# Optimization experiments

Measured on AMD Instinct MI355X. Metric: run time of the kernel, lower is better.

Reference implementation:

```python
import jax, jax.numpy as jnp
import numpy as np
from jax import lax

T = 8192
OBS = 512
HID = 2048
NOBJ = 8


def setup_inputs() -> dict:
    key = jax.random.key(0)
    ks = jax.random.split(key, 9)
    s_in = 1.0 / np.sqrt(OBS)
    s_hid = 1.0 / np.sqrt(HID)
    return {
        "x": jax.random.normal(ks[0], (T, OBS), dtype=jnp.float32),
        "W_in": jax.random.normal(ks[1], (HID, OBS), dtype=jnp.float32) * s_in,
        "W_B": jax.random.normal(ks[2], (HID, OBS), dtype=jnp.float32) * s_in,
        "W_C": jax.random.normal(ks[3], (HID, OBS), dtype=jnp.float32) * s_in,
        "W_delta": jax.random.normal(ks[4], (HID, OBS), dtype=jnp.float32) * s_in,
        "A_log": jax.random.normal(ks[5], (HID,), dtype=jnp.float32),
        "W_out": jax.random.normal(ks[6], (NOBJ, HID), dtype=jnp.float32) * s_hid,
        "b_out": jnp.zeros((NOBJ,), dtype=jnp.float32),
        "W_skip": jax.random.normal(ks[7], (NOBJ, OBS), dtype=jnp.float32) * s_in,
    }


def reference(x, W_in, W_B, W_C, W_delta, A_log, W_out, b_out, W_skip):
    # Input-dependent SSM parameters (4 GEMMs, [T, HID] each)
    x_state = x @ W_in.T
    B = x @ W_B.T
    C = x @ W_C.T
    delta = jax.nn.sigmoid(x @ W_delta.T)
    A = -jnp.exp(A_log)                      # [HID]

    A_bar = jnp.exp(delta * A)               # [T, HID], per-step decay
    Bx = B * x_state                         # [T, HID], per-step input

    def step(h, inp):
        a, bx = inp
        h = a * h + bx
        return h, h

    h0 = jnp.zeros((HID,), dtype=x.dtype)
    _, h_seq = lax.scan(step, h0, (A_bar, Bx))  # [T, HID]

    y = C * h_seq
    out = y @ W_out.T + b_out + x @ W_skip.T    # [T, NOBJ]
    return out
```

## Files before the change

### kernel.cpp

```cpp
#include <hip/hip_runtime.h>
#include <hip/hip_bf16.h>
#include <cstdint>

#define TT   8192
#define KOBS 512
#define HID  2048
#define NOBJ 8
#define NCH  64
#define CT   128

typedef unsigned short u16;
typedef uint32_t u32;
typedef short bf16x8 __attribute__((ext_vector_type(8)));
typedef float f32x4  __attribute__((ext_vector_type(4)));
typedef unsigned short u16x4 __attribute__((ext_vector_type(4)));

static __device__ __forceinline__ float bf2f(u16 u) {
    union { uint32_t i; float f; } v;
    v.i = ((uint32_t)u) << 16;
    return v.f;
}
static __device__ __forceinline__ u16 f2bf(float f) {
    union { float f; uint32_t i; } v;
    v.f = f;
    uint32_t lsb = (v.i >> 16) & 1u;
    uint32_t r = v.i + 0x7fffu + lsb;
    return (u16)(r >> 16);
}

static __device__ __forceinline__ void async_ld16(const u16* g, u16* l) {
    __builtin_amdgcn_global_load_lds(
        (const __attribute__((address_space(1))) uint32_t*)g,
        (__attribute__((address_space(3))) uint32_t*)l,
        16, 0, 0);
}

__global__ void prep_kernel(const float* __restrict__ x,
                            const float* __restrict__ Win,
                            const float* __restrict__ WB,
                            const float* __restrict__ WC,
                            const float* __restrict__ Wd,
                            const float* __restrict__ A_log,
                            u16* __restrict__ x_bf,
                            u16* __restrict__ W_bf,
                            float* __restrict__ A_e)
{
    const int tid0   = blockIdx.x * blockDim.x + threadIdx.x;
    const int stride = gridDim.x * blockDim.x;

    const float4* x4 = (const float4*)x;
    for (int i = tid0; i < TT * KOBS / 4; i += stride) {
        float4 v = x4[i];
        u16x4 o = { f2bf(v.x), f2bf(v.y), f2bf(v.z), f2bf(v.w) };
        *(u16x4*)&x_bf[(size_t)i * 4] = o;
    }

    for (int i = tid0; i < 4 * HID * KOBS / 8; i += stride) {
        int n  = i >> 6;
        int k8 = (i & 63) * 8;
        int h  = n >> 2;
        int w  = n & 3;
        const float* src = (w == 0) ? Win : (w == 1) ? WB : (w == 2) ? WC : Wd;
        const float4* s4 = (const float4*)(src + (size_t)h * KOBS + k8);
        float4 a = s4[0], b = s4[1];
        u16x4 o1 = { f2bf(a.x), f2bf(a.y), f2bf(a.z), f2bf(a.w) };
        u16x4 o2 = { f2bf(b.x), f2bf(b.y), f2bf(b.z), f2bf(b.w) };
        *(u16x4*)&W_bf[(size_t)i * 8]     = o1;
        *(u16x4*)&W_bf[(size_t)i * 8 + 4] = o2;
    }

    if (tid0 < HID)
        A_e[tid0] = -__expf(A_log[tid0]) * 1.44269504f;
}

__launch_bounds__(256)
__global__ void init_out(const float* __restrict__ x,
                         const float* __restrict__ b_out,
                         const float* __restrict__ W_skip,
                         float* __restrict__ out)
{
    const int wave = threadIdx.x >> 6;
    const int lane = threadIdx.x & 63;
    const int t0 = (blockIdx.x * 4 + wave) * 4;

    float acc[4][NOBJ];
#pragma unroll
    for (int tt = 0; tt < 4; tt++)
#pragma unroll
        for (int o = 0; o < NOBJ; o++) acc[tt][o] = 0.f;

#pragma unroll
    for (int i = 0; i < 2; i++) {
        const int kv = (i * 64 + lane) * 4;
        float4 w[NOBJ];
#pragma unroll
        for (int o = 0; o < NOBJ; o++)
            w[o] = *(const float4*)(W_skip + (size_t)o * KOBS + kv);
#pragma unroll
        for (int tt = 0; tt < 4; tt++) {
            float4 xv = *(const float4*)(x + (size_t)(t0 + tt) * KOBS + kv);
#pragma unroll
            for (int o = 0; o < NOBJ; o++)
                acc[tt][o] += xv.x * w[o].x + xv.y * w[o].y +
                              xv.z * w[o].z + xv.w * w[o].w;
        }
    }
#pragma unroll
    for (int s = 32; s > 0; s >>= 1)
#pragma unroll
        for (int tt = 0; tt < 4; tt++)
#pragma unroll
            for (int o = 0; o < NOBJ; o++)
                acc[tt][o] += __shfl_xor(acc[tt][o], s, 64);
    if (lane == 0) {
#pragma unroll
        for (int tt = 0; tt < 4; tt++)
#pragma unroll
            for (int o = 0; o < NOBJ; o++)
                out[(size_t)(t0 + tt) * NOBJ + o] = acc[tt][o] + b_out[o];
    }
}

__launch_bounds__(256)
__global__ void gemm_fused(const u16* __restrict__ x_bf,
                           const u16* __restrict__ W_bf,
                           const float* __restrict__ A_e,
                           u16* __restrict__ BX,
                           u16* __restrict__ CC,
                           u16* __restrict__ LA,
                           float* __restrict__ P,
                           float* __restrict__ S)
{
    __shared__ __align__(16) u16 smem[3 * 128 * 40];
    __shared__ float Ps[256], Ss[256];
    u16* a_s = smem;
    u16* b_s = smem + 4096;

    const int tid  = threadIdx.x;
    const int bm   = blockIdx.x & 63;
    const int bn   = blockIdx.x >> 6;
    const int m0t  = bm * 128;
    const int n0   = bn * 128;
    const int lane = tid & 63;
    const int wave = tid >> 6;
    const int wn   = (wave & 1) * 64;
    const int wt   = (wave >> 1) * 64;
    const int fr   = lane & 15;
    const int fq   = lane >> 4;

    f32x4 acc[4][4];
#pragma unroll
    for (int i = 0; i < 4; i++)
#pragma unroll
        for (int j = 0; j < 4; j++) {
            f32x4 z = {0.f, 0.f, 0.f, 0.f};
            acc[i][j] = z;
        }

    const int srow = tid >> 2;
    const int scg  = (tid & 3) ^ ((srow >> 1) & 3);
    const u16* gA0 = x_bf + (size_t)(m0t + srow) * KOBS + scg * 8;
    const u16* gA1 = gA0 + (size_t)64 * KOBS;
    const u16* gB0 = W_bf + (size_t)(n0 + srow) * KOBS + scg * 8;
    const u16* gB1 = gB0 + (size_t)64 * KOBS;
    u16* lA0 = &a_s[tid * 8];
    u16* lA1 = &a_s[2048 + tid * 8];
    u16* lB0 = &b_s[tid * 8];
    u16* lB1 = &b_s[2048 + tid * 8];

    const int pcg = fq ^ ((fr >> 1) & 3);

    for (int kb = 0; kb < KOBS; kb += 32) {
        async_ld16(gA0 + kb, lA0);
        async_ld16(gA1 + kb, lA1);
        async_ld16(gB0 + kb, lB0);
        async_ld16(gB1 + kb, lB1);
        __syncthreads();

        bf16x8 af[4], bfx[4];
#pragma unroll
        for (int i = 0; i < 4; i++)
            af[i] = *(const bf16x8*)&b_s[(wn + i * 16 + fr) * 32 + pcg * 8];
#pragma unroll
        for (int j = 0; j < 4; j++)
            bfx[j] = *(const bf16x8*)&a_s[(wt + j * 16 + fr) * 32 + pcg * 8];

#pragma unroll
        for (int i = 0; i < 4; i++)
#pragma unroll
            for (int j = 0; j < 4; j++)
                acc[i][j] = __builtin_amdgcn_mfma_f32_16x16x32_bf16(
                    af[i], bfx[j], acc[i][j], 0, 0, 0);
        __syncthreads();
    }

    const int hq = wn >> 2;
#pragma unroll
    for (int i = 0; i < 4; i++) {
        const int hl = hq + i * 4 + fq;
        const float ae = A_e[bn * 32 + hl];
#pragma unroll
        for (int j = 0; j < 4; j++) {
            const int tl = wt + j * 16 + fr;
            f32x4 v = acc[i][j];
            float sig = 1.0f / (1.0f + __expf(-v[3]));
            smem[(0 * 128 + tl) * 40 + hl] = f2bf(v[0] * v[1]);
            smem[(1 * 128 + tl) * 40 + hl] = f2bf(v[2]);
            smem[(2 * 128 + tl) * 40 + hl] = f2bf(sig * ae);
        }
    }
    __syncthreads();

#pragma unroll
    for (int it = 0; it < 6; it++) {
        const int g = it * 64 + (tid >> 2);
        const int a = g >> 7;
        const int t = g & 127;
        const int c = tid & 3;
        uint4 vd = *(const uint4*)&smem[(a * 128 + t) * 40 + c * 8];
        u16* dst = (a == 0 ? BX : (a == 1 ? CC : LA)) +
                   (size_t)(m0t + t) * HID + bn * 32 + c * 8;
        *(uint4*)dst = vd;
    }

    {
        const int hi  = tid & 31;
        const int seg = tid >> 5;
        float p = 1.f, s = 0.f;
        const int tbase = seg * 16;
#pragma unroll
        for (int t = 0; t < 16; t++) {
            float a  = exp2f(bf2f(smem[(2 * 128 + tbase + t) * 40 + hi]));
            float bx = bf2f(smem[(0 * 128 + tbase + t) * 40 + hi]);
            s = fmaf(a, s, bx);
            p *= a;
        }
        Ps[seg * 32 + hi] = p;
        Ss[seg * 32 + hi] = s;
        __syncthreads();
        if (tid < 32) {
            float pt = 1.f, st = 0.f;
#pragma unroll
            for (int sg = 0; sg < 8; sg++) {
                float ps = Ps[sg * 32 + tid], ss = Ss[sg * 32 + tid];
                st = fmaf(ps, st, ss);
                pt *= ps;
            }
            P[(size_t)bm * HID + bn * 32 + tid] = pt;
            S[(size_t)bm * HID + bn * 32 + tid] = st;
        }
    }
}

__global__ void scan_combine(const float* __restrict__ P,
                             const float* __restrict__ S,
                             float* __restrict__ H0)
{
    const int h = blockIdx.x * 256 + threadIdx.x;
    float hrun = 0.f;
#pragma unroll 8
    for (int c = 0; c < NCH; c++) {
        H0[c * HID + h] = hrun;
        hrun = fmaf(P[c * HID + h], hrun, S[c * HID + h]);
    }
}

__launch_bounds__(256)
__global__ void scan_out(const u16* __restrict__ LA,
                         const u16* __restrict__ BX,
                         const u16* __restrict__ CC,
                         const float* __restrict__ H0,
                         const float* __restrict__ W_out,
                         float* __restrict__ out)
{
    __shared__ __align__(16) u16 ybuf[128 * 256];
    __shared__ float wst[8 * 260];
    const int tid  = threadIdx.x;
    const int c    = blockIdx.x >> 3;
    const int hg   = blockIdx.x & 7;
    const int lane = tid & 63;
    const int wave = tid >> 6;
    const int fr   = lane & 15;
    const int fq   = lane >> 4;

#pragma unroll
    for (int o = 0; o < 8; o++)
        wst[o * 260 + tid] = W_out[(size_t)o * HID + hg * 256 + tid];

    const int h = hg * 256 + tid;
    float hrun = H0[c * HID + h];
    size_t base = ((size_t)c * CT) * HID + h;
    const int g  = tid >> 3;
    const int lo = tid & 7;
    for (int tb = 0; tb < CT; tb += 4) {
        u16 la4[4], bx4[4], cc4[4];
#pragma unroll
        for (int q = 0; q < 4; q++) {
            la4[q] = LA[base + (size_t)q * HID];
            bx4[q] = BX[base + (size_t)q * HID];
            cc4[q] = CC[base + (size_t)q * HID];
        }
#pragma unroll
        for (int q = 0; q < 4; q++) {
            float a = exp2f(bf2f(la4[q]));
            hrun = fmaf(a, hrun, bf2f(bx4[q]));
            const int t = tb + q;
            ybuf[t * 256 + (((g ^ (t & 7)) << 3) | lo)] = f2bf(bf2f(cc4[q]) * hrun);
        }
        base += (size_t)4 * HID;
    }
    __syncthreads();

    bf16x8 bw[8];
#pragma unroll
    for (int ks = 0; ks < 8; ks++) {
        bf16x8 w;
#pragma unroll
        for (int j = 0; j < 8; j++) {
            u16 v = (fr < 8) ? f2bf(wst[fr * 260 + ks * 32 + fq * 8 + j])
                             : (u16)0;
            w[j] = (short)v;
        }
        bw[ks] = w;
    }

#pragma unroll
    for (int mt = 0; mt < 2; mt++) {
        const int tb = wave * 32 + mt * 16;
        const int t  = tb + fr;
        f32x4 acc2 = {0.f, 0.f, 0.f, 0.f};
#pragma unroll
        for (int ks = 0; ks < 8; ks++) {
            const int gg = ks * 4 + fq;
            bf16x8 yv = *(const bf16x8*)
                &ybuf[t * 256 + ((gg ^ (fr & 7)) << 3)];
            acc2 = __builtin_amdgcn_mfma_f32_16x16x32_bf16(bw[ks], yv, acc2,
                                                           0, 0, 0);
        }
        if (fq < 2) {
            const int tg = c * CT + tb + fr;
#pragma unroll
            for (int reg = 0; reg < 4; reg++)
                atomicAdd(&out[(size_t)tg * NOBJ + 4 * fq + reg], acc2[reg]);
        }
    }
}

extern "C" void kernel_launch(void* const* d_in, const int* in_sizes, int n_in,
                              void* d_out, int out_size, void* d_ws, size_t ws_size,
                              hipStream_t stream)
{
    const float* x      = (const float*)d_in[0];
    const float* Win    = (const float*)d_in[1];
    const float* WB     = (const float*)d_in[2];
    const float* WC     = (const float*)d_in[3];
    const float* Wd     = (const float*)d_in[4];
    const float* A_log  = (const float*)d_in[5];
    const float* W_out  = (const float*)d_in[6];
    const float* b_out  = (const float*)d_in[7];
    const float* W_skip = (const float*)d_in[8];
    float* out = (float*)d_out;

    char* ws = (char*)d_ws;
    size_t off = 0;
    auto alloc = [&](size_t bytes) -> void* {
        void* p = (void*)(ws + off);
        off += (bytes + 255) & ~(size_t)255;
        return p;
    };

    u16*   x_bf = (u16*)  alloc((size_t)TT * KOBS * 2);
    u16*   W_bf = (u16*)  alloc((size_t)4 * HID * KOBS * 2);
    float* A_e  = (float*)alloc((size_t)HID * 4);
    u16*   LA   = (u16*)  alloc((size_t)TT * HID * 2);
    u16*   BX   = (u16*)  alloc((size_t)TT * HID * 2);
    u16*   CC   = (u16*)  alloc((size_t)TT * HID * 2);
    float* P    = (float*)alloc((size_t)NCH * HID * 4);
    float* S    = (float*)alloc((size_t)NCH * HID * 4);
    float* H0   = (float*)alloc((size_t)NCH * HID * 4);
    (void)ws_size; (void)in_sizes; (void)n_in; (void)out_size;

    prep_kernel<<<2048, 256, 0, stream>>>(x, Win, WB, WC, Wd, A_log,
                                          x_bf, W_bf, A_e);
    init_out<<<512, 256, 0, stream>>>(x, b_out, W_skip, out);
    gemm_fused<<<4096, 256, 0, stream>>>(x_bf, W_bf, A_e, BX, CC, LA, P, S);
    scan_combine<<<8, 256, 0, stream>>>(P, S, H0);
    scan_out<<<512, 256, 0, stream>>>(LA, BX, CC, H0, W_out, out);
}
```

Before: 222.0 us.

## Interleave scan operands into one buffer, halve chunk length, fuse x conversion

Measured after the change: 229.6 us. +3.4%, slower.

```diff
diff --git a/kernel.cpp b/kernel.cpp
--- a/kernel.cpp
+++ b/kernel.cpp
@@ -6,8 +6,8 @@
 #define KOBS 512
 #define HID  2048
 #define NOBJ 8
-#define NCH  64
-#define CT   128
+#define NCH  128
+#define CT   64
 
 typedef unsigned short u16;
 typedef uint32_t u32;
@@ -35,25 +35,16 @@
         16, 0, 0);
 }
 
-__global__ void prep_kernel(const float* __restrict__ x,
-                            const float* __restrict__ Win,
-                            const float* __restrict__ WB,
-                            const float* __restrict__ WC,
-                            const float* __restrict__ Wd,
-                            const float* __restrict__ A_log,
-                            u16* __restrict__ x_bf,
-                            u16* __restrict__ W_bf,
-                            float* __restrict__ A_e)
+__global__ void prep_w(const float* __restrict__ Win,
+                       const float* __restrict__ WB,
+                       const float* __restrict__ WC,
+                       const float* __restrict__ Wd,
+                       const float* __restrict__ A_log,
+                       u16* __restrict__ W_bf,
+                       float* __restrict__ A_e)
 {
     const int tid0   = blockIdx.x * blockDim.x + threadIdx.x;
     const int stride = gridDim.x * blockDim.x;
-
-    const float4* x4 = (const float4*)x;
-    for (int i = tid0; i < TT * KOBS / 4; i += stride) {
-        float4 v = x4[i];
-        u16x4 o = { f2bf(v.x), f2bf(v.y), f2bf(v.z), f2bf(v.w) };
-        *(u16x4*)&x_bf[(size_t)i * 4] = o;
-    }
 
     for (int i = tid0; i < 4 * HID * KOBS / 8; i += stride) {
         int n  = i >> 6;
@@ -74,10 +65,11 @@
 }
 
 __launch_bounds__(256)
-__global__ void init_out(const float* __restrict__ x,
-                         const float* __restrict__ b_out,
-                         const float* __restrict__ W_skip,
-                         float* __restrict__ out)
+__global__ void prep_x_out(const float* __restrict__ x,
+                           const float* __restrict__ b_out,
+                           const float* __restrict__ W_skip,
+                           float* __restrict__ out,
+                           u16* __restrict__ x_bf)
 {
     const int wave = threadIdx.x >> 6;
     const int lane = threadIdx.x & 63;
@@ -98,7 +90,10 @@
             w[o] = *(const float4*)(W_skip + (size_t)o * KOBS + kv);
 #pragma unroll
         for (int tt = 0; tt < 4; tt++) {
-            float4 xv = *(const float4*)(x + (size_t)(t0 + tt) * KOBS + kv);
+            const size_t off = (size_t)(t0 + tt) * KOBS + kv;
+            float4 xv = *(const float4*)(x + off);
+            u16x4 xb = { f2bf(xv.x), f2bf(xv.y), f2bf(xv.z), f2bf(xv.w) };
+            *(u16x4*)&x_bf[off] = xb;
 #pragma unroll
             for (int o = 0; o < NOBJ; o++)
                 acc[tt][o] += xv.x * w[o].x + xv.y * w[o].y +
@@ -125,13 +120,11 @@
 __global__ void gemm_fused(const u16* __restrict__ x_bf,
                            const u16* __restrict__ W_bf,
                            const float* __restrict__ A_e,
-                           u16* __restrict__ BX,
-                           u16* __restrict__ CC,
-                           u16* __restrict__ LA,
+                           u16* __restrict__ G,
                            float* __restrict__ P,
                            float* __restrict__ S)
 {
-    __shared__ __align__(16) u16 smem[3 * 128 * 40];
+    __shared__ __align__(16) u16 smem[128 * 37 * 4];
     __shared__ float Ps[256], Ss[256];
     u16* a_s = smem;
     u16* b_s = smem + 4096;
@@ -204,23 +197,22 @@
             const int tl = wt + j * 16 + fr;
             f32x4 v = acc[i][j];
             float sig = 1.0f / (1.0f + __expf(-v[3]));
-            smem[(0 * 128 + tl) * 40 + hl] = f2bf(v[0] * v[1]);
-            smem[(1 * 128 + tl) * 40 + hl] = f2bf(v[2]);
-            smem[(2 * 128 + tl) * 40 + hl] = f2bf(sig * ae);
+            u32 lo = (u32)f2bf(v[0] * v[1]) | ((u32)f2bf(v[2]) << 16);
+            u32 hi = (u32)f2bf(sig * ae);
+            *(uint2*)&smem[(tl * 37 + hl) * 4] = make_uint2(lo, hi);
         }
     }
     __syncthreads();
 
 #pragma unroll
-    for (int it = 0; it < 6; it++) {
-        const int g = it * 64 + (tid >> 2);
-        const int a = g >> 7;
-        const int t = g & 127;
-        const int c = tid & 3;
-        uint4 vd = *(const uint4*)&smem[(a * 128 + t) * 40 + c * 8];
-        u16* dst = (a == 0 ? BX : (a == 1 ? CC : LA)) +
-                   (size_t)(m0t + t) * HID + bn * 32 + c * 8;
-        *(uint4*)dst = vd;
+    for (int it = 0; it < 8; it++) {
+        const int g   = it * 256 + tid;
+        const int row = g >> 4;
+        const int c2  = g & 15;
+        uint2 lo = *(const uint2*)&smem[(row * 37 + c2 * 2) * 4];
+        uint2 hi = *(const uint2*)&smem[(row * 37 + c2 * 2 + 1) * 4];
+        uint4 v = make_uint4(lo.x, lo.y, hi.x, hi.y);
+        *(uint4*)(G + ((size_t)(m0t + row) * HID + bn * 32 + c2 * 2) * 4) = v;
     }
 
     {
@@ -230,24 +222,27 @@
         const int tbase = seg * 16;
 #pragma unroll
         for (int t = 0; t < 16; t++) {
-            float a  = exp2f(bf2f(smem[(2 * 128 + tbase + t) * 40 + hi]));
-            float bx = bf2f(smem[(0 * 128 + tbase + t) * 40 + hi]);
+            uint2 w = *(const uint2*)&smem[((tbase + t) * 37 + hi) * 4];
+            float a  = exp2f(bf2f((u16)(w.y & 0xffff)));
+            float bx = bf2f((u16)(w.x & 0xffff));
             s = fmaf(a, s, bx);
             p *= a;
         }
         Ps[seg * 32 + hi] = p;
         Ss[seg * 32 + hi] = s;
         __syncthreads();
-        if (tid < 32) {
+        if (tid < 64) {
+            const int half = tid >> 5, h2 = tid & 31;
             float pt = 1.f, st = 0.f;
 #pragma unroll
-            for (int sg = 0; sg < 8; sg++) {
-                float ps = Ps[sg * 32 + tid], ss = Ss[sg * 32 + tid];
+            for (int sg = 0; sg < 4; sg++) {
+                float ps = Ps[(half * 4 + sg) * 32 + h2];
+                float ss = Ss[(half * 4 + sg) * 32 + h2];
                 st = fmaf(ps, st, ss);
                 pt *= ps;
             }
-            P[(size_t)bm * HID + bn * 32 + tid] = pt;
-            S[(size_t)bm * HID + bn * 32 + tid] = st;
+            P[(size_t)(bm * 2 + half) * HID + bn * 32 + h2] = pt;
+            S[(size_t)(bm * 2 + half) * HID + bn * 32 + h2] = st;
         }
     }
 }
@@ -266,15 +261,13 @@
 }
 
 __launch_bounds__(256)
-__global__ void scan_out(const u16* __restrict__ LA,
-                         const u16* __restrict__ BX,
-                         const u16* __restrict__ CC,
+__global__ void scan_out(const u16* __restrict__ G,
                          const float* __restrict__ H0,
                          const float* __restrict__ W_out,
                          float* __restrict__ out)
 {
-    __shared__ __align__(16) u16 ybuf[128 * 256];
-    __shared__ float wst[8 * 260];
+    __shared__ __align__(16) u16 ybuf[CT * 256];
+    __shared__ __align__(16) u16 wst[8 * 264];
     const int tid  = threadIdx.x;
     const int c    = blockIdx.x >> 3;
     const int hg   = blockIdx.x & 7;
@@ -285,48 +278,42 @@
 
 #pragma unroll
     for (int o = 0; o < 8; o++)
-        wst[o * 260 + tid] = W_out[(size_t)o * HID + hg * 256 + tid];
+        wst[o * 264 + tid] = f2bf(W_out[(size_t)o * HID + hg * 256 + tid]);
 
     const int h = hg * 256 + tid;
     float hrun = H0[c * HID + h];
-    size_t base = ((size_t)c * CT) * HID + h;
+    size_t base = (size_t)c * CT * HID + h;
     const int g  = tid >> 3;
     const int lo = tid & 7;
-    for (int tb = 0; tb < CT; tb += 4) {
-        u16 la4[4], bx4[4], cc4[4];
-#pragma unroll
-        for (int q = 0; q < 4; q++) {
-            la4[q] = LA[base + (size_t)q * HID];
-            bx4[q] = BX[base + (size_t)q * HID];
-            cc4[q] = CC[base + (size_t)q * HID];
-        }
-#pragma unroll
-        for (int q = 0; q < 4; q++) {
-            float a = exp2f(bf2f(la4[q]));
-            hrun = fmaf(a, hrun, bf2f(bx4[q]));
+    for (int tb = 0; tb < CT; tb += 8) {
+        uint2 wv[8];
+#pragma unroll
+        for (int q = 0; q < 8; q++)
+            wv[q] = *(const uint2*)&G[(base + (size_t)q * HID) * 4];
+#pragma unroll
+        for (int q = 0; q < 8; q++) {
+            float bx = bf2f((u16)(wv[q].x & 0xffff));
+            float cc = bf2f((u16)(wv[q].x >> 16));
+            float a  = exp2f(bf2f((u16)(wv[q].y & 0xffff)));
+            hrun = fmaf(a, hrun, bx);
             const int t = tb + q;
-            ybuf[t * 256 + (((g ^ (t & 7)) << 3) | lo)] = f2bf(bf2f(cc4[q]) * hrun);
-        }
-        base += (size_t)4 * HID;
+            ybuf[t * 256 + (((g ^ (t & 7)) << 3) | lo)] = f2bf(cc * hrun);
+        }
+        base += (size_t)8 * HID;
     }
     __syncthreads();
 
     bf16x8 bw[8];
 #pragma unroll
     for (int ks = 0; ks < 8; ks++) {
-        bf16x8 w;
-#pragma unroll
-        for (int j = 0; j < 8; j++) {
-            u16 v = (fr < 8) ? f2bf(wst[fr * 260 + ks * 32 + fq * 8 + j])
-                             : (u16)0;
-            w[j] = (short)v;
-        }
+        bf16x8 w = {0, 0, 0, 0, 0, 0, 0, 0};
+        if (fr < 8)
+            w = *(const bf16x8*)&wst[fr * 264 + ks * 32 + fq * 8];
         bw[ks] = w;
     }
 
-#pragma unroll
-    for (int mt = 0; mt < 2; mt++) {
-        const int tb = wave * 32 + mt * 16;
+    {
+        const int tb = wave * 16;
         const int t  = tb + fr;
         f32x4 acc2 = {0.f, 0.f, 0.f, 0.f};
 #pragma unroll
@@ -338,7 +325,7 @@
                                                            0, 0, 0);
         }
         if (fq < 2) {
-            const int tg = c * CT + tb + fr;
+            const int tg = c * CT + t;
 #pragma unroll
             for (int reg = 0; reg < 4; reg++)
                 atomicAdd(&out[(size_t)tg * NOBJ + 4 * fq + reg], acc2[reg]);
@@ -372,18 +359,15 @@
     u16*   x_bf = (u16*)  alloc((size_t)TT * KOBS * 2);
     u16*   W_bf = (u16*)  alloc((size_t)4 * HID * KOBS * 2);
     float* A_e  = (float*)alloc((size_t)HID * 4);
-    u16*   LA   = (u16*)  alloc((size_t)TT * HID * 2);
-    u16*   BX   = (u16*)  alloc((size_t)TT * HID * 2);
-    u16*   CC   = (u16*)  alloc((size_t)TT * HID * 2);
+    u16*   G    = (u16*)  alloc((size_t)TT * HID * 8);
     float* P    = (float*)alloc((size_t)NCH * HID * 4);
     float* S    = (float*)alloc((size_t)NCH * HID * 4);
     float* H0   = (float*)alloc((size_t)NCH * HID * 4);
     (void)ws_size; (void)in_sizes; (void)n_in; (void)out_size;
 
-    prep_kernel<<<2048, 256, 0, stream>>>(x, Win, WB, WC, Wd, A_log,
-                                          x_bf, W_bf, A_e);
-    init_out<<<512, 256, 0, stream>>>(x, b_out, W_skip, out);
-    gemm_fused<<<4096, 256, 0, stream>>>(x_bf, W_bf, A_e, BX, CC, LA, P, S);
+    prep_w<<<2048, 256, 0, stream>>>(Win, WB, WC, Wd, A_log, W_bf, A_e);
+    prep_x_out<<<512, 256, 0, stream>>>(x, b_out, W_skip, out, x_bf);
+    gemm_fused<<<4096, 256, 0, stream>>>(x_bf, W_bf, A_e, G, P, S);
     scan_combine<<<8, 256, 0, stream>>>(P, S, H0);
-    scan_out<<<512, 256, 0, stream>>>(LA, BX, CC, H0, W_out, out);
-}
+    scan_out<<<1024, 256, 0, stream>>>(G, H0, W_out, out);
+}
```
